# Kernel optimization log

Measured on AMD Instinct MI355X. Metric: run time of the kernel, lower is better.

Reference implementation:

```python
import jax, jax.numpy as jnp
import numpy as np

B, T, HID = 1, 256, 2048
H, D = 16, 128
KD = H * D
CONV = 4
MAX_CG = 30
LAMB_LB = 0.25
NORM_EPS = 1e-5


def setup_inputs() -> dict:
    key = jax.random.key(0)
    ks = jax.random.split(key, 10)
    s = 0.02
    init_lamb = float(np.log(np.exp(1.0 - LAMB_LB) - 1.0))  # softplus^-1(1 - lower_bound)
    return {
        "hidden_states": jax.random.normal(ks[0], (B, T, HID), jnp.float32),
        "Wq": jax.random.normal(ks[1], (HID, KD), jnp.float32) * s,
        "Wk": jax.random.normal(ks[2], (HID, KD), jnp.float32) * s,
        "Wv": jax.random.normal(ks[3], (HID, KD), jnp.float32) * s,
        "Wa": jax.random.normal(ks[4], (HID, H), jnp.float32) * s,
        "ba": jnp.full((H,), 2.0, jnp.float32),
        "Wb": jax.random.normal(ks[5], (HID, H), jnp.float32) * s,
        "bb": jnp.zeros((H,), jnp.float32),
        "conv_wq": jax.random.normal(ks[6], (KD, CONV), jnp.float32) * s,
        "conv_wk": jax.random.normal(ks[7], (KD, CONV), jnp.float32) * s,
        "lambda_params": jnp.full((KD,), init_lamb, jnp.float32),
        "o_norm_w": jnp.ones((D,), jnp.float32),
        "Wo": jax.random.normal(ks[8], (KD, HID), jnp.float32) * s,
    }


def short_conv_silu(x, w):
    # depthwise causal conv over time; x [b,t,c], w [c,k]
    k = w.shape[1]
    xp = jnp.pad(x, ((0, 0), (k - 1, 0), (0, 0)))
    t = x.shape[1]
    y = xp[:, 0:t, :] * w[:, 0]
    for i in range(1, k):
        y = y + xp[:, i:i + t, :] * w[:, i]
    return jax.nn.silu(y)


def l2norm(x):
    return x * jax.lax.rsqrt(jnp.sum(x * x, -1, keepdims=True) + 1e-6)


def rmsnorm(x, w):
    return x * jax.lax.rsqrt(jnp.mean(x * x, -1, keepdims=True) + NORM_EPS) * w


def cg_solve(A, b):
    # solve A x = b per (batch, head) with fixed CG iterations, x0 = 0
    matvec = lambda p: jnp.einsum('bhij,bhj->bhi', A, p)
    x0 = jnp.zeros_like(b)
    rs0 = jnp.sum(b * b, -1)

    def body(i, st):
        xc, r, p, rs = st
        Ap = matvec(p)
        alpha = rs / (jnp.sum(p * Ap, -1) + 1e-12)
        xc = xc + alpha[..., None] * p
        r = r - alpha[..., None] * Ap
        rs_n = jnp.sum(r * r, -1)
        p = r + (rs_n / (rs + 1e-12))[..., None] * p
        return xc, r, p, rs_n

    xf, _, _, _ = jax.lax.fori_loop(0, MAX_CG, body, (x0, b, b, rs0))
    return xf


def mesa_recurrence(q, k, v, g, beta, lamb_diag):
    # q,k,v [b,t,h,d]; g,beta [b,t,h]; lamb_diag [h,d,d]
    def step(carry, inp):
        h_kk, h_kv = carry
        qt, kt, vt, gt, bt = inp
        decay = jnp.exp(gt)[..., None, None]
        b_ = bt[..., None, None]
        h_kk = h_kk * decay + b_ * (kt[..., :, None] * kt[..., None, :])
        h_kv = h_kv * decay + b_ * (kt[..., :, None] * vt[..., None, :])
        A = h_kk + lamb_diag[None]
        q_star = cg_solve(A, qt)
        ot = jnp.einsum('bhk,bhkv->bhv', q_star, h_kv)
        return (h_kk, h_kv), ot

    init = (jnp.zeros((B, H, D, D), q.dtype), jnp.zeros((B, H, D, D), q.dtype))
    xs = (q.transpose(1, 0, 2, 3), k.transpose(1, 0, 2, 3), v.transpose(1, 0, 2, 3),
          g.transpose(1, 0, 2), beta.transpose(1, 0, 2))
    _, o = jax.lax.scan(step, init, xs)
    return o.transpose(1, 0, 2, 3)  # [b,t,h,d]


def reference(hidden_states, Wq, Wk, Wv, Wa, ba, Wb, bb, conv_wq, conv_wk,
              lambda_params, o_norm_w, Wo):
    x = hidden_states
    q = short_conv_silu(x @ Wq, conv_wq)
    k = short_conv_silu(x @ Wk, conv_wk)
    v = x @ Wv
    q = l2norm(q.reshape(B, T, H, D))
    k = l2norm(k.reshape(B, T, H, D))
    v = v.reshape(B, T, H, D)
    beta = jax.nn.sigmoid(x @ Wb + bb)          # [b,t,h]
    g = jax.nn.log_sigmoid(x @ Wa + ba)          # [b,t,h]
    lamb = (jax.nn.softplus(lambda_params) + LAMB_LB).reshape(H, D)
    lamb_diag = lamb[:, :, None] * jnp.eye(D, dtype=lamb.dtype)  # [h,d,d]
    o = mesa_recurrence(q, k, v, g, beta, lamb_diag)
    o = rmsnorm(o, o_norm_w)
    o = o.reshape(B, T, KD) @ Wo
    return o
```

## Files before the change

### kernel.cpp

```cpp
#include <hip/hip_runtime.h>
#include <math.h>

#define TT 256
#define HIDDEN 2048
#define NH 16
#define HD 128
#define KDIM 2048
#define NCG 30

typedef _Float16 h4 __attribute__((ext_vector_type(4)));
typedef _Float16 half8 __attribute__((ext_vector_type(8)));
typedef float floatx4 __attribute__((ext_vector_type(4)));

__device__ __forceinline__ half8 cvt8(const float4 x, const float4 y) {
    half8 f;
    f[0] = (_Float16)x.x; f[1] = (_Float16)x.y; f[2] = (_Float16)x.z; f[3] = (_Float16)x.w;
    f[4] = (_Float16)y.x; f[5] = (_Float16)y.y; f[6] = (_Float16)y.z; f[7] = (_Float16)y.w;
    return f;
}

__device__ __forceinline__ void glds16(const void* g, void* l) {
    __builtin_amdgcn_global_load_lds(
        (const __attribute__((address_space(1))) void*)g,
        (__attribute__((address_space(3))) void*)l, 16, 0, 0);
}

#define ASTR 72
#define GEMM_LDS (2 * 64 * 128 * 4 + 2 * 64 * ASTR * 2)

__global__ __launch_bounds__(256) void gemm_kernel(
    const float* __restrict__ A,
    const float* __restrict__ Wq, const float* __restrict__ Wk,
    const float* __restrict__ Wv,
    const float* __restrict__ Wa, const float* __restrict__ Wb,
    float* __restrict__ C0, float* __restrict__ C1, float* __restrict__ C2,
    const float* __restrict__ ba, const float* __restrict__ bb,
    float* __restrict__ g, float* __restrict__ beta)
{
    extern __shared__ char smem[];
    float* Bf = (float*)smem;
    _Float16* Ash = (_Float16*)(smem + 65536);

    const int tid = threadIdx.x, lane = tid & 63, w = tid >> 6;
    const int q = lane >> 4, l16 = lane & 15;

    const int b = blockIdx.x;
    const int xcd = b & 7, gslot = b >> 3;
    int nt, mt;
    if (gslot < 24) { nt = xcd * 6 + (gslot >> 2); mt = gslot & 3; }
    else           { nt = 48;                      mt = xcd; }
    const int mat = nt >> 4;
    const int ntile = nt & 15;
    const int n0 = ntile * 128;
    const float* __restrict__ W = (mat == 0) ? Wq : (mat == 1) ? Wk : (mat == 2) ? Wv : Wa;
    float* __restrict__ C = (mat == 0) ? C0 : (mat == 1) ? C1 : C2;
    const int m0 = mt * 64;

    const int ar = tid >> 2, ac = (tid & 3) * 16;
    const float* __restrict__ Ap = &A[(size_t)(m0 + ar) * KDIM + ac];

    floatx4 acc[4][2] = {};
    float4 a0, a1, a2, a3;
    float bab[16];

    auto stageB = [&](int s, int buf) {
#pragma unroll
        for (int i = 0; i < 8; i++) {
            const int r0 = w * 16 + i * 2;
            const int row = r0 + (lane >> 5);
            glds16(&W[(size_t)(s * 64 + row) * KDIM + n0 + (lane & 31) * 4],
                   &Bf[(buf * 64 + r0) * 128]);
        }
    };
    auto loadBab = [&](int s) {
        if (w >= 2) return;
        const float* __restrict__ Wsrc = (w == 0) ? Wa : Wb;
        const int hh = lane & 15, ko = lane >> 4;
#pragma unroll
        for (int hf = 0; hf < 2; hf++)
#pragma unroll
            for (int j = 0; j < 8; j++)
                bab[hf * 8 + j] = Wsrc[(size_t)(s * 64 + hf * 32 + ko * 8 + j) * NH + hh];
    };
    auto writeBab = [&](int buf) {
        if (w >= 2) return;
        const int hh = lane & 15, ko = lane >> 4;
        const int col = w * 16 + hh;
#pragma unroll
        for (int hf = 0; hf < 2; hf++)
#pragma unroll
            for (int j = 0; j < 8; j++)
                Bf[(buf * 64 + hf * 32 + ko * 8 + j) * 128 + col] = bab[hf * 8 + j];
    };

    if (mat == 3) {
        for (int i = tid; i < 2 * 64 * 96; i += 256) {
            const int buf = i / 6144;
            const int rest = i - buf * 6144;
            const int row = rest / 96, col = 32 + (rest - row * 96);
            Bf[(buf * 64 + row) * 128 + col] = 0.f;
        }
        loadBab(0); writeBab(0); loadBab(1);
    } else {
        stageB(0, 0);
    }
    a0 = *(const float4*)&Ap[0]; a1 = *(const float4*)&Ap[4];
    a2 = *(const float4*)&Ap[8]; a3 = *(const float4*)&Ap[12];
    *(half8*)&Ash[ar * ASTR + ac] = cvt8(a0, a1);
    *(half8*)&Ash[ar * ASTR + ac + 8] = cvt8(a2, a3);
    a0 = *(const float4*)&Ap[64]; a1 = *(const float4*)&Ap[68];
    a2 = *(const float4*)&Ap[72]; a3 = *(const float4*)&Ap[76];
    __syncthreads();

    const int NSTEP = KDIM / 64;
    for (int s = 0; s < NSTEP; s++) {
        const int cur = s & 1;
        if (mat != 3 && s + 1 < NSTEP)
            stageB(s + 1, cur ^ 1);
#pragma unroll
        for (int kk = 0; kk < 2; kk++) {
            float f0[8], f1[8];
#pragma unroll
            for (int j = 0; j < 8; j++) {
                const int rowb = (cur * 64 + kk * 32 + q * 8 + j) * 128 + w * 32 + l16;
                f0[j] = Bf[rowb];
                f1[j] = Bf[rowb + 16];
            }
            const half8 bf0 = cvt8(*(const float4*)&f0[0], *(const float4*)&f0[4]);
            const half8 bf1 = cvt8(*(const float4*)&f1[0], *(const float4*)&f1[4]);
#pragma unroll
            for (int rr = 0; rr < 4; rr++) {
                const half8 af = *(const half8*)&Ash[cur * 64 * ASTR + (rr * 16 + l16) * ASTR + kk * 32 + q * 8];
                acc[rr][0] = __builtin_amdgcn_mfma_f32_16x16x32_f16(af, bf0, acc[rr][0], 0, 0, 0);
                acc[rr][1] = __builtin_amdgcn_mfma_f32_16x16x32_f16(af, bf1, acc[rr][1], 0, 0, 0);
            }
        }
        if (s + 1 < NSTEP) {
            if (mat == 3) {
                writeBab(cur ^ 1);
                if (s + 2 < NSTEP) loadBab(s + 2);
            }
            *(half8*)&Ash[(cur ^ 1) * 64 * ASTR + ar * ASTR + ac] = cvt8(a0, a1);
            *(half8*)&Ash[(cur ^ 1) * 64 * ASTR + ar * ASTR + ac + 8] = cvt8(a2, a3);
            if (s + 2 < NSTEP) {
                a0 = *(const float4*)&Ap[(s + 2) * 64];      a1 = *(const float4*)&Ap[(s + 2) * 64 + 4];
                a2 = *(const float4*)&Ap[(s + 2) * 64 + 8];  a3 = *(const float4*)&Ap[(s + 2) * 64 + 12];
            }
        }
        __syncthreads();
    }

    if (mat == 3) {
        if (w == 0) {
            const float bav = ba[l16], bbv = bb[l16];
#pragma unroll
            for (int rr = 0; rr < 4; rr++)
#pragma unroll
                for (int r = 0; r < 4; r++) {
                    const int tr = m0 + rr * 16 + q * 4 + r;
                    float z0 = acc[rr][0][r] + bav;
                    g[tr * NH + l16] = fminf(z0, 0.f) - log1pf(__expf(-fabsf(z0)));
                    float z1 = acc[rr][1][r] + bbv;
                    beta[tr * NH + l16] = 1.f / (1.f + __expf(-z1));
                }
        }
        return;
    }

#pragma unroll
    for (int rr = 0; rr < 4; rr++)
#pragma unroll
        for (int r = 0; r < 4; r++) {
            const int row = m0 + rr * 16 + q * 4 + r;
            C[(size_t)row * KDIM + n0 + w * 32 + l16] = acc[rr][0][r];
            C[(size_t)row * KDIM + n0 + w * 32 + 16 + l16] = acc[rr][1][r];
        }
}

__global__ __launch_bounds__(256) void gemm64_kernel(
    const float* __restrict__ A, const float* __restrict__ Wo,
    float* __restrict__ C)
{
    __shared__ __align__(16) float Bf[2][64][64];
    __shared__ __align__(16) _Float16 Ash[2][32 * ASTR];

    const int tid = threadIdx.x, lane = tid & 63, w = tid >> 6;
    const int q = lane >> 4, l16 = lane & 15;
    const int b = blockIdx.x;
    const int xcd = b & 7, gslot = b >> 3;
    const int nt = xcd * 4 + (gslot >> 3), mt = gslot & 7;
    const int n0 = nt * 64, m0 = mt * 32;

    const int ar = tid >> 3, ac = (tid & 7) * 8;
    const float* __restrict__ Ap = &A[(size_t)(m0 + ar) * KDIM + ac];

    floatx4 acc0 = {}, acc1 = {};
    float4 ax, ay;

    auto stageB = [&](int s, int buf) {
#pragma unroll
        for (int i = 0; i < 4; i++) {
            const int r0 = w * 16 + i * 4;
            const int row = r0 + (lane >> 4);
            glds16(&Wo[(size_t)(s * 64 + row) * KDIM + n0 + (lane & 15) * 4],
                   &Bf[buf][r0][0]);
        }
    };

    stageB(0, 0);
    ax = *(const float4*)&Ap[0]; ay = *(const float4*)&Ap[4];
    *(half8*)&Ash[0][ar * ASTR + ac] = cvt8(ax, ay);
    ax = *(const float4*)&Ap[64]; ay = *(const float4*)&Ap[68];
    __syncthreads();

    const int NSTEP = KDIM / 64;
    for (int s = 0; s < NSTEP; s++) {
        const int cur = s & 1;
        if (s + 1 < NSTEP) stageB(s + 1, cur ^ 1);
#pragma unroll
        for (int kk = 0; kk < 2; kk++) {
            float f[8];
#pragma unroll
            for (int j = 0; j < 8; j++)
                f[j] = Bf[cur][kk * 32 + q * 8 + j][w * 16 + l16];
            const half8 bf  = cvt8(*(const float4*)&f[0], *(const float4*)&f[4]);
            const half8 af0 = *(const half8*)&Ash[cur][l16 * ASTR + kk * 32 + q * 8];
            const half8 af1 = *(const half8*)&Ash[cur][(16 + l16) * ASTR + kk * 32 + q * 8];
            acc0 = __builtin_amdgcn_mfma_f32_16x16x32_f16(af0, bf, acc0, 0, 0, 0);
            acc1 = __builtin_amdgcn_mfma_f32_16x16x32_f16(af1, bf, acc1, 0, 0, 0);
        }
        if (s + 1 < NSTEP) {
            *(half8*)&Ash[cur ^ 1][ar * ASTR + ac] = cvt8(ax, ay);
            if (s + 2 < NSTEP) {
                ax = *(const float4*)&Ap[(s + 2) * 64];
                ay = *(const float4*)&Ap[(s + 2) * 64 + 4];
            }
        }
        __syncthreads();
    }

#pragma unroll
    for (int r = 0; r < 4; r++) {
        C[(size_t)(m0 + q * 4 + r) * KDIM + n0 + w * 16 + l16] = acc0[r];
        C[(size_t)(m0 + 16 + q * 4 + r) * KDIM + n0 + w * 16 + l16] = acc1[r];
    }
}

__global__ __launch_bounds__(256) void conv_silu_l2_kernel(
    const float* __restrict__ q_pre, const float* __restrict__ k_pre,
    const float* __restrict__ cwq, const float* __restrict__ cwk,
    float* __restrict__ qn, float* __restrict__ kn)
{
    const int t = blockIdx.x, h = blockIdx.y;
    const int which = threadIdx.x >> 7, d = threadIdx.x & 127;
    const int w = threadIdx.x >> 6;
    const int c = h * HD + d;
    const float* pre = which ? k_pre : q_pre;
    const float* cw  = which ? cwk : cwq;
    float y = 0.f;
#pragma unroll
    for (int i = 0; i < 4; i++) {
        const int ts = t - 3 + i;
        if (ts >= 0) y = fmaf(pre[ts * KDIM + c], cw[c * 4 + i], y);
    }
    const float s = y / (1.f + __expf(-y));
    float v = s * s;
#pragma unroll
    for (int off = 32; off > 0; off >>= 1) v += __shfl_down(v, off, 64);
    __shared__ float red[4];
    if ((threadIdx.x & 63) == 0) red[w] = v;
    __syncthreads();
    const float sum = red[which * 2] + red[which * 2 + 1];
    float* dst = which ? kn : qn;
    dst[t * KDIM + c] = s * rsqrtf(sum + 1e-6f);
}

#define PSTR 136
#define YSTR 264

template<int SMAX>
__device__ __forceinline__ void mesa_cg(
    const float* __restrict__ qn, const float* __restrict__ kn, const float* __restrict__ vv,
    const float* __restrict__ g, const float* __restrict__ bet, const float* __restrict__ lp,
    const float* __restrict__ onw, float* __restrict__ out,
    int h, int t0, _Float16* Psh, _Float16* Ysh, float* red,
    float* Gsh, float* bets)
{
    constexpr int NSUB1 = SMAX / 64;
    constexpr int NK2   = SMAX / 32;

    const int tid = threadIdx.x, lane = tid & 63, w = tid >> 6;
    const int quad = lane >> 4, l16 = lane & 15;
    const int tmy = t0 + l16;
    const int dbase = w * 32;

    {
        float sc = g[tid * NH + h];
#pragma unroll
        for (int off = 1; off < 64; off <<= 1) {
            const float o = __shfl_up(sc, off, 64);
            if (lane >= off) sc += o;
        }
        if (lane == 63) red[w] = sc;
        bets[tid] = bet[tid * NH + h];
        __syncthreads();
        float woff = 0.f;
        for (int u = 0; u < w; u++) woff += red[u];
        Gsh[tid] = sc + woff;
        __syncthreads();
    }

    half8 K1[NSUB1][4];
#pragma unroll
    for (int ii = 0; ii < NSUB1; ii++) {
        const int srow = 16 * (w + 4 * ii) + l16;
        const float* kp = &kn[(srow * NH + h) * HD];
#pragma unroll
        for (int kk = 0; kk < 4; kk++) {
            const float4 a = *(const float4*)&kp[kk * 32 + quad * 8];
            const float4 b = *(const float4*)&kp[kk * 32 + quad * 8 + 4];
            K1[ii][kk] = cvt8(a, b);
        }
    }

    half8 KtF[2][NK2];
#pragma unroll
    for (int ss = 0; ss < 2; ss++) {
        const int d = dbase + ss * 16 + l16;
#pragma unroll
        for (int kk = 0; kk < NK2; kk++) {
#pragma unroll
            for (int j = 0; j < 8; j++) {
                const int s = kk * 32 + quad * 8 + j;
                KtF[ss][kk][j] = (_Float16)kn[(s * NH + h) * HD + d];
            }
        }
    }

    half8 Vf[NK2][2];
#pragma unroll
    for (int kk = 0; kk < NK2; kk++) {
#pragma unroll
        for (int ss = 0; ss < 2; ss++) {
            const int dv = dbase + ss * 16 + l16;
#pragma unroll
            for (int j = 0; j < 8; j++) {
                const int s = kk * 32 + quad * 8 + j;
                Vf[kk][ss][j] = (_Float16)vv[(s * NH + h) * HD + dv];
            }
        }
    }

    const float Gt = Gsh[tmy];
    float Wm[NSUB1][4];
#pragma unroll
    for (int ii = 0; ii < NSUB1; ii++)
#pragma unroll
        for (int r = 0; r < 4; r++) {
            const int s = 16 * (w + 4 * ii) + quad * 4 + r;
            Wm[ii][r] = (s <= tmy) ? bets[s] * __expf(Gt - Gsh[s]) : 0.f;
        }
    float lam[8], xv[8], rv[8], pv[8];
#pragma unroll
    for (int ss = 0; ss < 2; ss++)
#pragma unroll
        for (int r = 0; r < 4; r++) {
            const int e = ss * 4 + r;
            const int d = dbase + ss * 16 + quad * 4 + r;
            const float lx = lp[h * HD + d];
            lam[e] = fmaxf(lx, 0.f) + log1pf(__expf(-fabsf(lx))) + 0.25f;
            const float b = qn[(tmy * NH + h) * HD + d];
            xv[e] = 0.f; rv[e] = b; pv[e] = b;
        }
    float rs = 0.f;
#pragma unroll
    for (int e = 0; e < 8; e++) rs += rv[e] * rv[e];
    rs += __shfl_xor(rs, 16, 64); rs += __shfl_xor(rs, 32, 64);

    auto writeP = [&](const float* src) {
#pragma unroll
        for (int ss = 0; ss < 2; ss++) {
            h4 ph;
            ph.x = (_Float16)src[ss * 4 + 0]; ph.y = (_Float16)src[ss * 4 + 1];
            ph.z = (_Float16)src[ss * 4 + 2]; ph.w = (_Float16)src[ss * 4 + 3];
            *(h4*)&Psh[l16 * PSTR + dbase + ss * 16 + quad * 4] = ph;
        }
    };
    writeP(pv);

    for (int it = 0; it <= NCG; it++) {
        __syncthreads();
        floatx4 acc1a[NSUB1] = {}, acc1b[NSUB1] = {};
#pragma unroll
        for (int kk = 0; kk < 2; kk++) {
            const half8 bfa = *(const half8*)&Psh[l16 * PSTR + kk * 32 + quad * 8];
            const half8 bfb = *(const half8*)&Psh[l16 * PSTR + (kk + 2) * 32 + quad * 8];
#pragma unroll
            for (int ii = 0; ii < NSUB1; ii++) {
                acc1a[ii] = __builtin_amdgcn_mfma_f32_16x16x32_f16(K1[ii][kk], bfa, acc1a[ii], 0, 0, 0);
                acc1b[ii] = __builtin_amdgcn_mfma_f32_16x16x32_f16(K1[ii][kk + 2], bfb, acc1b[ii], 0, 0, 0);
            }
        }
#pragma unroll
        for (int ii = 0; ii < NSUB1; ii++) {
            h4 yh;
            yh.x = (_Float16)(Wm[ii][0] * (acc1a[ii][0] + acc1b[ii][0]));
            yh.y = (_Float16)(Wm[ii][1] * (acc1a[ii][1] + acc1b[ii][1]));
            yh.z = (_Float16)(Wm[ii][2] * (acc1a[ii][2] + acc1b[ii][2]));
            yh.w = (_Float16)(Wm[ii][3] * (acc1a[ii][3] + acc1b[ii][3]));
            *(h4*)&Ysh[l16 * YSTR + 16 * (w + 4 * ii) + quad * 4] = yh;
        }
        __syncthreads();
        if (it == NCG) break;

        floatx4 acc2a[2] = {}, acc2b[2] = {};
#pragma unroll
        for (int kk = 0; kk < NK2; kk += 2) {
            const half8 bf0 = *(const half8*)&Ysh[l16 * YSTR + kk * 32 + quad * 8];
            const half8 bf1 = *(const half8*)&Ysh[l16 * YSTR + (kk + 1) * 32 + quad * 8];
#pragma unroll
            for (int ss = 0; ss < 2; ss++) {
                acc2a[ss] = __builtin_amdgcn_mfma_f32_16x16x32_f16(KtF[ss][kk], bf0, acc2a[ss], 0, 0, 0);
                acc2b[ss] = __builtin_amdgcn_mfma_f32_16x16x32_f16(KtF[ss][kk + 1], bf1, acc2b[ss], 0, 0, 0);
            }
        }
        float Ap[8], pAp = 0.f;
#pragma unroll
        for (int ss = 0; ss < 2; ss++)
#pragma unroll
            for (int r = 0; r < 4; r++) {
                const int e = ss * 4 + r;
                Ap[e] = (acc2a[ss][r] + acc2b[ss][r]) + lam[e] * pv[e];
                pAp = fmaf(pv[e], Ap[e], pAp);
            }
        pAp += __shfl_xor(pAp, 16, 64); pAp += __shfl_xor(pAp, 32, 64);
        const float alpha = rs / (pAp + 1e-12f);
        float rsn = 0.f;
#pragma unroll
        for (int e = 0; e < 8; e++) {
            xv[e] = fmaf(alpha, pv[e], xv[e]);
            rv[e] = fmaf(-alpha, Ap[e], rv[e]);
            rsn = fmaf(rv[e], rv[e], rsn);
        }
        rsn += __shfl_xor(rsn, 16, 64); rsn += __shfl_xor(rsn, 32, 64);
        const float bcg = rsn / (rs + 1e-12f);
#pragma unroll
        for (int e = 0; e < 8; e++) pv[e] = fmaf(bcg, pv[e], rv[e]);
        rs = rsn;
        writeP(it == NCG - 1 ? xv : pv);
    }

    floatx4 accOa[2] = {}, accOb[2] = {};
#pragma unroll
    for (int kk = 0; kk < NK2; kk += 2) {
        const half8 af0 = *(const half8*)&Ysh[l16 * YSTR + kk * 32 + quad * 8];
        const half8 af1 = *(const half8*)&Ysh[l16 * YSTR + (kk + 1) * 32 + quad * 8];
#pragma unroll
        for (int ss = 0; ss < 2; ss++) {
            accOa[ss] = __builtin_amdgcn_mfma_f32_16x16x32_f16(af0, Vf[kk][ss], accOa[ss], 0, 0, 0);
            accOb[ss] = __builtin_amdgcn_mfma_f32_16x16x32_f16(af1, Vf[kk + 1][ss], accOb[ss], 0, 0, 0);
        }
    }
    float accO[2][4];
#pragma unroll
    for (int ss = 0; ss < 2; ss++)
#pragma unroll
        for (int r = 0; r < 4; r++) accO[ss][r] = accOa[ss][r] + accOb[ss][r];

    float part[4];
#pragma unroll
    for (int r = 0; r < 4; r++) {
        part[r] = accO[0][r] * accO[0][r] + accO[1][r] * accO[1][r];
#pragma unroll
        for (int off = 1; off < 16; off <<= 1) part[r] += __shfl_xor(part[r], off, 64);
    }
    if (l16 == 0) {
#pragma unroll
        for (int r = 0; r < 4; r++) red[w * 16 + quad * 4 + r] = part[r];
    }
    __syncthreads();
    const float w0 = onw[dbase + l16], w1 = onw[dbase + 16 + l16];
#pragma unroll
    for (int r = 0; r < 4; r++) {
        const int qr = quad * 4 + r;
        const float sumd = red[qr] + red[16 + qr] + red[32 + qr] + red[48 + qr];
        const float sc = rsqrtf(sumd * (1.f / HD) + 1e-5f);
        const int trow = ((t0 + qr) * NH + h) * HD;
        out[trow + dbase + l16] = accO[0][r] * sc * w0;
        out[trow + dbase + 16 + l16] = accO[1][r] * sc * w1;
    }
}

__global__ __launch_bounds__(256, 1) void mesa_kernel(
    const float* __restrict__ qn, const float* __restrict__ kn, const float* __restrict__ vv,
    const float* __restrict__ g, const float* __restrict__ bet, const float* __restrict__ lp,
    const float* __restrict__ onw, float* __restrict__ out)
{
    __shared__ __align__(16) _Float16 Psh[16 * PSTR];
    __shared__ __align__(16) _Float16 Ysh[16 * YSTR];
    __shared__ float red[64];
    __shared__ float Gsh[256];
    __shared__ float bets[256];
    const int h = blockIdx.x, jb = blockIdx.y, t0 = jb * 16;
    switch (jb >> 2) {
        case 0:  mesa_cg<64> (qn, kn, vv, g, bet, lp, onw, out, h, t0, Psh, Ysh, red, Gsh, bets); break;
        case 1:  mesa_cg<128>(qn, kn, vv, g, bet, lp, onw, out, h, t0, Psh, Ysh, red, Gsh, bets); break;
        case 2:  mesa_cg<192>(qn, kn, vv, g, bet, lp, onw, out, h, t0, Psh, Ysh, red, Gsh, bets); break;
        default: mesa_cg<256>(qn, kn, vv, g, bet, lp, onw, out, h, t0, Psh, Ysh, red, Gsh, bets); break;
    }
}

extern "C" void kernel_launch(void* const* d_in, const int* in_sizes, int n_in,
                              void* d_out, int out_size, void* d_ws, size_t ws_size,
                              hipStream_t stream)
{
    (void)in_sizes; (void)n_in; (void)out_size; (void)ws_size;
    const float* x   = (const float*)d_in[0];
    const float* Wq  = (const float*)d_in[1];
    const float* Wk  = (const float*)d_in[2];
    const float* Wv  = (const float*)d_in[3];
    const float* Wa  = (const float*)d_in[4];
    const float* ba  = (const float*)d_in[5];
    const float* Wb  = (const float*)d_in[6];
    const float* bb  = (const float*)d_in[7];
    const float* cwq = (const float*)d_in[8];
    const float* cwk = (const float*)d_in[9];
    const float* lp  = (const float*)d_in[10];
    const float* onw = (const float*)d_in[11];
    const float* Wo  = (const float*)d_in[12];

    char* wsb = (char*)d_ws;
    float* q_pre = (float*)wsb;
    float* k_pre = q_pre + 524288;
    float* v     = k_pre + 524288;
    float* qn    = v + 524288;
    float* kn    = qn + 524288;
    float* g     = kn + 524288;
    float* beta  = g + 4096;
    float* onorm = q_pre;
    float* outp  = (float*)d_out;

    (void)hipFuncSetAttribute((const void*)gemm_kernel,
                              hipFuncAttributeMaxDynamicSharedMemorySize, GEMM_LDS);
    gemm_kernel<<<dim3(196), 256, GEMM_LDS, stream>>>(x, Wq, Wk, Wv, Wa, Wb,
                                                      q_pre, k_pre, v, ba, bb, g, beta);
    conv_silu_l2_kernel<<<dim3(TT, NH), 256, 0, stream>>>(q_pre, k_pre, cwq, cwk, qn, kn);

    mesa_kernel<<<dim3(NH, 16), 256, 0, stream>>>(qn, kn, v, g, beta, lp, onw, onorm);

    gemm64_kernel<<<dim3(256), 256, 0, stream>>>(onorm, Wo, outp);
}
```

Before: 229.5 us.

## Triple-buffer weight tiles in GEMMs with explicit waitcnt and single barrier

Both projection GEMMs move from double- to triple-buffered LDS for the weight tiles, prefetching two k-steps ahead via global_load_lds. Each iteration now uses a single barrier guarded by manual s_waitcnt vmcnt counts and sched_barrier fences, so weight loads overlap with MFMA compute instead of stalling on a trailing __syncthreads. The cost is more LDS per block, which may lower occupancy, and the hand-set vmcnt values are fragile: they must match the exact number of outstanding loads per thread.

Measured after the change: 230.8 us. Within noise of the previous version (+0.6%).

```diff
diff --git a/kernel.cpp b/kernel.cpp
--- a/kernel.cpp
+++ b/kernel.cpp
@@ -25,8 +25,10 @@
         (__attribute__((address_space(3))) void*)l, 16, 0, 0);
 }
 
+#define SBAR() __builtin_amdgcn_sched_barrier(0)
+
 #define ASTR 72
-#define GEMM_LDS (2 * 64 * 128 * 4 + 2 * 64 * ASTR * 2)
+#define GEMM_LDS (3 * 64 * 128 * 4 + 2 * 64 * ASTR * 2)
 
 __global__ __launch_bounds__(256) void gemm_kernel(
     const float* __restrict__ A,
@@ -39,7 +41,7 @@
 {
     extern __shared__ char smem[];
     float* Bf = (float*)smem;
-    _Float16* Ash = (_Float16*)(smem + 65536);
+    _Float16* Ash = (_Float16*)(smem + 3 * 64 * 128 * 4);
 
     const int tid = threadIdx.x, lane = tid & 63, w = tid >> 6;
     const int q = lane >> 4, l16 = lane & 15;
@@ -72,6 +74,14 @@
                    &Bf[(buf * 64 + r0) * 128]);
         }
     };
+    auto loadA = [&](int s) {
+        a0 = *(const float4*)&Ap[s * 64];      a1 = *(const float4*)&Ap[s * 64 + 4];
+        a2 = *(const float4*)&Ap[s * 64 + 8];  a3 = *(const float4*)&Ap[s * 64 + 12];
+    };
+    auto writeA = [&](int buf) {
+        *(half8*)&Ash[buf * 64 * ASTR + ar * ASTR + ac] = cvt8(a0, a1);
+        *(half8*)&Ash[buf * 64 * ASTR + ar * ASTR + ac + 8] = cvt8(a2, a3);
+    };
     auto loadBab = [&](int s) {
         if (w >= 2) return;
         const float* __restrict__ Wsrc = (w == 0) ? Wa : Wb;
@@ -92,6 +102,28 @@
             for (int j = 0; j < 8; j++)
                 Bf[(buf * 64 + hf * 32 + ko * 8 + j) * 128 + col] = bab[hf * 8 + j];
     };
+
+    const int NSTEP = KDIM / 64;
+
+#define GEMM_COMPUTE(BBASE, ABASE)                                                          \
+    _Pragma("unroll")                                                                       \
+    for (int kk = 0; kk < 2; kk++) {                                                        \
+        float f0[8], f1[8];                                                                 \
+        _Pragma("unroll")                                                                   \
+        for (int j = 0; j < 8; j++) {                                                       \
+            const int rowb = ((BBASE) + kk * 32 + q * 8 + j) * 128 + w * 32 + l16;          \
+            f0[j] = Bf[rowb];                                                               \
+            f1[j] = Bf[rowb + 16];                                                          \
+        }                                                                                   \
+        const half8 bf0 = cvt8(*(const float4*)&f0[0], *(const float4*)&f0[4]);             \
+        const half8 bf1 = cvt8(*(const float4*)&f1[0], *(const float4*)&f1[4]);             \
+        _Pragma("unroll")                                                                   \
+        for (int rr = 0; rr < 4; rr++) {                                                    \
+            const half8 af = *(const half8*)&Ash[(ABASE) + (rr * 16 + l16) * ASTR + kk * 32 + q * 8]; \
+            acc[rr][0] = __builtin_amdgcn_mfma_f32_16x16x32_f16(af, bf0, acc[rr][0], 0, 0, 0); \
+            acc[rr][1] = __builtin_amdgcn_mfma_f32_16x16x32_f16(af, bf1, acc[rr][1], 0, 0, 0); \
+        }                                                                                   \
+    }
 
     if (mat == 3) {
         for (int i = tid; i < 2 * 64 * 96; i += 256) {
@@ -101,56 +133,19 @@
             Bf[(buf * 64 + row) * 128 + col] = 0.f;
         }
         loadBab(0); writeBab(0); loadBab(1);
-    } else {
-        stageB(0, 0);
-    }
-    a0 = *(const float4*)&Ap[0]; a1 = *(const float4*)&Ap[4];
-    a2 = *(const float4*)&Ap[8]; a3 = *(const float4*)&Ap[12];
-    *(half8*)&Ash[ar * ASTR + ac] = cvt8(a0, a1);
-    *(half8*)&Ash[ar * ASTR + ac + 8] = cvt8(a2, a3);
-    a0 = *(const float4*)&Ap[64]; a1 = *(const float4*)&Ap[68];
-    a2 = *(const float4*)&Ap[72]; a3 = *(const float4*)&Ap[76];
-    __syncthreads();
-
-    const int NSTEP = KDIM / 64;
-    for (int s = 0; s < NSTEP; s++) {
-        const int cur = s & 1;
-        if (mat != 3 && s + 1 < NSTEP)
-            stageB(s + 1, cur ^ 1);
-#pragma unroll
-        for (int kk = 0; kk < 2; kk++) {
-            float f0[8], f1[8];
-#pragma unroll
-            for (int j = 0; j < 8; j++) {
-                const int rowb = (cur * 64 + kk * 32 + q * 8 + j) * 128 + w * 32 + l16;
-                f0[j] = Bf[rowb];
-                f1[j] = Bf[rowb + 16];
-            }
-            const half8 bf0 = cvt8(*(const float4*)&f0[0], *(const float4*)&f0[4]);
-            const half8 bf1 = cvt8(*(const float4*)&f1[0], *(const float4*)&f1[4]);
-#pragma unroll
-            for (int rr = 0; rr < 4; rr++) {
-                const half8 af = *(const half8*)&Ash[cur * 64 * ASTR + (rr * 16 + l16) * ASTR + kk * 32 + q * 8];
-                acc[rr][0] = __builtin_amdgcn_mfma_f32_16x16x32_f16(af, bf0, acc[rr][0], 0, 0, 0);
-                acc[rr][1] = __builtin_amdgcn_mfma_f32_16x16x32_f16(af, bf1, acc[rr][1], 0, 0, 0);
-            }
-        }
-        if (s + 1 < NSTEP) {
-            if (mat == 3) {
+        loadA(0); writeA(0); loadA(1);
+        __syncthreads();
+        for (int s = 0; s < NSTEP; s++) {
+            const int cur = s & 1;
+            GEMM_COMPUTE(cur * 64, cur * 64 * ASTR);
+            if (s + 1 < NSTEP) {
                 writeBab(cur ^ 1);
                 if (s + 2 < NSTEP) loadBab(s + 2);
+                writeA(cur ^ 1);
+                if (s + 2 < NSTEP) loadA(s + 2);
             }
-            *(half8*)&Ash[(cur ^ 1) * 64 * ASTR + ar * ASTR + ac] = cvt8(a0, a1);
-            *(half8*)&Ash[(cur ^ 1) * 64 * ASTR + ar * ASTR + ac + 8] = cvt8(a2, a3);
-            if (s + 2 < NSTEP) {
-                a0 = *(const float4*)&Ap[(s + 2) * 64];      a1 = *(const float4*)&Ap[(s + 2) * 64 + 4];
-                a2 = *(const float4*)&Ap[(s + 2) * 64 + 8];  a3 = *(const float4*)&Ap[(s + 2) * 64 + 12];
-            }
-        }
-        __syncthreads();
-    }
-
-    if (mat == 3) {
+            __syncthreads();
+        }
         if (w == 0) {
             const float bav = ba[l16], bbv = bb[l16];
 #pragma unroll
@@ -167,6 +162,27 @@
         return;
     }
 
+    stageB(0, 0);
+    SBAR();
+    loadA(0); writeA(0);
+    SBAR();
+    stageB(1, 1);
+    SBAR();
+    loadA(1);
+
+    for (int s = 0; s < NSTEP; s++) {
+        if (s < NSTEP - 1) { asm volatile("s_waitcnt vmcnt(16) lgkmcnt(0)" ::: "memory"); }
+        else               { asm volatile("s_waitcnt vmcnt(0) lgkmcnt(0)" ::: "memory"); }
+        SBAR();
+        __builtin_amdgcn_s_barrier();
+        SBAR();
+        if (s + 2 < NSTEP) stageB(s + 2, (s + 2) % 3);
+        SBAR();
+        if (s + 1 < NSTEP) writeA((s + 1) & 1);
+        if (s + 2 < NSTEP) loadA(s + 2);
+        GEMM_COMPUTE((s % 3) * 64, (s & 1) * 64 * ASTR);
+    }
+
 #pragma unroll
     for (int rr = 0; rr < 4; rr++)
 #pragma unroll
@@ -175,13 +191,14 @@
             C[(size_t)row * KDIM + n0 + w * 32 + l16] = acc[rr][0][r];
             C[(size_t)row * KDIM + n0 + w * 32 + 16 + l16] = acc[rr][1][r];
         }
+#undef GEMM_COMPUTE
 }
 
 __global__ __launch_bounds__(256) void gemm64_kernel(
     const float* __restrict__ A, const float* __restrict__ Wo,
     float* __restrict__ C)
 {
-    __shared__ __align__(16) float Bf[2][64][64];
+    __shared__ __align__(16) float Bf[3][64][64];
     __shared__ __align__(16) _Float16 Ash[2][32 * ASTR];
 
     const int tid = threadIdx.x, lane = tid & 63, w = tid >> 6;
@@ -206,37 +223,46 @@
                    &Bf[buf][r0][0]);
         }
     };
+    auto loadA = [&](int s) {
+        ax = *(const float4*)&Ap[s * 64];
+        ay = *(const float4*)&Ap[s * 64 + 4];
+    };
+    auto writeA = [&](int buf) {
+        *(half8*)&Ash[buf][ar * ASTR + ac] = cvt8(ax, ay);
+    };
 
     stageB(0, 0);
-    ax = *(const float4*)&Ap[0]; ay = *(const float4*)&Ap[4];
-    *(half8*)&Ash[0][ar * ASTR + ac] = cvt8(ax, ay);
-    ax = *(const float4*)&Ap[64]; ay = *(const float4*)&Ap[68];
-    __syncthreads();
+    SBAR();
+    loadA(0); writeA(0);
+    SBAR();
+    stageB(1, 1);
+    SBAR();
+    loadA(1);
 
     const int NSTEP = KDIM / 64;
     for (int s = 0; s < NSTEP; s++) {
-        const int cur = s & 1;
-        if (s + 1 < NSTEP) stageB(s + 1, cur ^ 1);
+        if (s < NSTEP - 1) { asm volatile("s_waitcnt vmcnt(8) lgkmcnt(0)" ::: "memory"); }
+        else               { asm volatile("s_waitcnt vmcnt(0) lgkmcnt(0)" ::: "memory"); }
+        SBAR();
+        __builtin_amdgcn_s_barrier();
+        SBAR();
+        if (s + 2 < NSTEP) stageB(s + 2, (s + 2) % 3);
+        SBAR();
+        if (s + 1 < NSTEP) writeA((s + 1) & 1);
+        if (s + 2 < NSTEP) loadA(s + 2);
+        const int bb = s % 3, ab = s & 1;
 #pragma unroll
         for (int kk = 0; kk < 2; kk++) {
             float f[8];
 #pragma unroll
             for (int j = 0; j < 8; j++)
-                f[j] = Bf[cur][kk * 32 + q * 8 + j][w * 16 + l16];
+                f[j] = Bf[bb][kk * 32 + q * 8 + j][w * 16 + l16];
             const half8 bf  = cvt8(*(const float4*)&f[0], *(const float4*)&f[4]);
-            const half8 af0 = *(const half8*)&Ash[cur][l16 * ASTR + kk * 32 + q * 8];
-            const half8 af1 = *(const half8*)&Ash[cur][(16 + l16) * ASTR + kk * 32 + q * 8];
+            const half8 af0 = *(const half8*)&Ash[ab][l16 * ASTR + kk * 32 + q * 8];
+            const half8 af1 = *(const half8*)&Ash[ab][(16 + l16) * ASTR + kk * 32 + q * 8];
             acc0 = __builtin_amdgcn_mfma_f32_16x16x32_f16(af0, bf, acc0, 0, 0, 0);
             acc1 = __builtin_amdgcn_mfma_f32_16x16x32_f16(af1, bf, acc1, 0, 0, 0);
         }
-        if (s + 1 < NSTEP) {
-            *(half8*)&Ash[cur ^ 1][ar * ASTR + ac] = cvt8(ax, ay);
-            if (s + 2 < NSTEP) {
-                ax = *(const float4*)&Ap[(s + 2) * 64];
-                ay = *(const float4*)&Ap[(s + 2) * 64 + 4];
-            }
-        }
-        __syncthreads();
     }
 
 #pragma unroll
```
